# Optimization experiments

Hardware: AMD Instinct MI355X
Metric: run time of the kernel (lower is better)

## Reference

```python
import jax, jax.numpy as jnp
import numpy as np
from jax import lax

EOS_ID = 2
START_ID = 1
NEG = -1e9
BEAM = 4
OUT_LEN = 48


def _lstm_gates(z):
    i, f, g, o = jnp.split(z, 4, axis=-1)
    return jax.nn.sigmoid(i), jax.nn.sigmoid(f), jnp.tanh(g), jax.nn.sigmoid(o)


def setup_inputs() -> dict:
    V, E, H, A = 32000, 512, 512, 512
    B, S_IN = 32, 128
    key = jax.random.key(0)
    ks = jax.random.split(key, 16)
    sd = 0.05
    n = lambda k, shp: jax.random.normal(k, shp, dtype=jnp.float32) * sd
    return {
        "encoder_inputs": jax.random.randint(ks[0], (B, S_IN), 0, V, dtype=jnp.int32),
        "decoder_inputs": jax.random.randint(ks[1], (B, OUT_LEN), 0, V, dtype=jnp.int32),
        "enc_emb": n(ks[2], (V, E)),
        "dec_emb": n(ks[3], (V, E)),
        "W_enc": n(ks[4], (E, 4 * H)),
        "U_enc": n(ks[5], (H, 4 * H)),
        "b_enc": jnp.zeros((4 * H,), jnp.float32),
        "W_dec": n(ks[6], (E + A, 4 * H)),
        "U_dec": n(ks[7], (H, 4 * H)),
        "b_dec": jnp.zeros((4 * H,), jnp.float32),
        "W_mem": n(ks[8], (H, A)),      # LuongAttention memory layer (no bias)
        "W_attn": n(ks[9], (2 * H, A)), # AttentionWrapper attention layer (no bias)
        "W_out": n(ks[10], (A, V)),
        "b_out": jnp.zeros((V,), jnp.float32),
    }


def reference(encoder_inputs, decoder_inputs, enc_emb, dec_emb, W_enc, U_enc, b_enc,
              W_dec, U_dec, b_dec, W_mem, W_attn, W_out, b_out):
    B = encoder_inputs.shape[0]
    H = U_enc.shape[0]
    A = W_mem.shape[1]
    V = W_out.shape[1]

    # ---- encoder LSTM (Keras gate order i,f,g,o) ----
    x = enc_emb[encoder_inputs]  # [B,S,E]
    def enc_step(carry, xt):
        h, c = carry
        i, f, g, o = _lstm_gates(xt @ W_enc + h @ U_enc + b_enc)
        c = f * c + i * g
        h = o * jnp.tanh(c)
        return (h, c), h
    h0 = jnp.zeros((B, H), x.dtype)
    (hN, cN), enc_out = lax.scan(enc_step, (h0, h0), x.transpose(1, 0, 2))
    enc_out = enc_out.transpose(1, 0, 2)       # [B,S,H] = attention values
    keys_mem = enc_out @ W_mem                 # [B,S,A] = attention keys

    # ---- beam search init (tile encoder final state over beams) ----
    h = jnp.broadcast_to(hN[:, None], (B, BEAM, H))
    c = jnp.broadcast_to(cN[:, None], (B, BEAM, H))
    attn = jnp.zeros((B, BEAM, A), x.dtype)
    cum = jnp.full((B, BEAM), NEG, x.dtype).at[:, 0].set(0.0)
    finished = jnp.zeros((B, BEAM), bool)
    tok = jnp.full((B, BEAM), START_ID, jnp.int32)
    eos_lp = jnp.full((V,), NEG, x.dtype).at[EOS_ID].set(0.0)

    def dec_step(carry, _):
        h, c, attn, cum, finished, tok = carry
        xe = dec_emb[tok]                                     # [B,K,E]
        inp = jnp.concatenate([xe, attn], axis=-1)            # cell_input_fn: concat(input, attention)
        i, f, g, o = _lstm_gates(inp @ W_dec + h @ U_dec + b_dec)
        c_new = f * c + i * g
        cell_out = o * jnp.tanh(c_new)                        # [B,K,H]
        scores = jnp.einsum('bkh,bsh->bks', cell_out, keys_mem)  # Luong dot score
        align = jax.nn.softmax(scores, axis=-1)
        ctx = jnp.einsum('bks,bsh->bkh', align, enc_out)
        attn_new = jnp.concatenate([cell_out, ctx], axis=-1) @ W_attn  # attention layer
        logits = attn_new @ W_out + b_out                     # [B,K,V]
        lp = jax.nn.log_softmax(logits, axis=-1)
        lp = jnp.where(finished[..., None], eos_lp, lp)       # finished beams repeat EOS
        total = cum[..., None] + lp
        vals, idx = lax.top_k(total.reshape(B, -1), BEAM)     # over K*V candidates
        parent = idx // V
        new_tok = (idx % V).astype(jnp.int32)
        g3 = lambda t: jnp.take_along_axis(t, parent[..., None], axis=1)
        h2 = g3(cell_out)
        c2 = g3(c_new)
        attn2 = g3(attn_new)
        fin = jnp.take_along_axis(finished, parent, axis=1) | (new_tok == EOS_ID)
        return (h2, c2, attn2, vals, fin, new_tok), (parent, new_tok)

    _, (parents, toks) = lax.scan(dec_step, (h, c, attn, cum, finished, tok), None, length=OUT_LEN)

    # ---- gather_tree: backtrack beam ancestry ----
    def back(ptr, pt):
        p, t = pt
        sel = jnp.take_along_axis(t, ptr, axis=1)
        return jnp.take_along_axis(p, ptr, axis=1), sel
    ptr0 = jnp.broadcast_to(jnp.arange(BEAM, dtype=jnp.int32)[None], (B, BEAM))
    _, pred = lax.scan(back, ptr0, (parents, toks), reverse=True)
    return pred.transpose(1, 0, 2)  # predicted_ids [B, T, beam]
```

## Files before the change

### kernel.cpp

```cpp
#include <hip/hip_runtime.h>
#include <math.h>

#define EOS_ID 2
#define START_ID 1
#define NEGV (-1e9f)

__device__ __forceinline__ float sigmoidf_(float x) { return 1.f / (1.f + expf(-x)); }

__device__ __forceinline__ void merge4_(float lv[4], int lc[4],
                                        const float rv[4], const int rc[4]) {
    float ov[4]; int oc[4];
    int ai = 0, bi = 0;
    #pragma unroll
    for (int o = 0; o < 4; o++) {
        const float avv = (ai == 0) ? lv[0] : (ai == 1) ? lv[1] : (ai == 2) ? lv[2] : lv[3];
        const int   acc = (ai == 0) ? lc[0] : (ai == 1) ? lc[1] : (ai == 2) ? lc[2] : lc[3];
        const float bvv = (bi == 0) ? rv[0] : (bi == 1) ? rv[1] : (bi == 2) ? rv[2] : rv[3];
        const int   bcc = (bi == 0) ? rc[0] : (bi == 1) ? rc[1] : (bi == 2) ? rc[2] : rc[3];
        const bool ta = (avv > bvv) || (avv == bvv && acc < bcc);
        ov[o] = ta ? avv : bvv;
        oc[o] = ta ? acc : bcc;
        if (ta) ai++; else bi++;
    }
    #pragma unroll
    for (int o = 0; o < 4; o++) { lv[o] = ov[o]; lc[o] = oc[o]; }
}

__device__ __forceinline__ void lse_combine_(float& m, float& s, float m2, float s2) {
    const float M = fmaxf(m, m2);
    s = s * expf(m - M) + s2 * expf(m2 - M);
    m = M;
}

template<int BM, int BN, int BK, int AMODE, int TRANS>
__global__ void __launch_bounds__(256) gemm_k(
    const float* __restrict__ A, const float* __restrict__ B,
    const float* __restrict__ bias, float* __restrict__ C,
    int M, int N, int K, const int* __restrict__ tokp)
{
    static_assert(BN == 64, "");
    constexpr int TM = BM / 16, TN = BN / 16;
    __shared__ __align__(16) float As[BK][BM];
    __shared__ __align__(16) float Bs[BK][BN];
    const int tid = threadIdx.x;
    const int n0 = blockIdx.x * BN, m0 = blockIdx.y * BM;
    const int tx = tid & 15, ty = tid >> 4;
    (void)M;

    float acc[TM][TN];
    #pragma unroll
    for (int i = 0; i < TM; i++)
        #pragma unroll
        for (int j = 0; j < TN; j++) acc[i][j] = 0.f;

    constexpr int A4 = BM * BK / 4;
    const bool aP = (A4 >= 256) || (tid < A4);
    const int am = tid / (BK / 4), ak4 = tid % (BK / 4);
    const int bk = tid >> 4, bn4 = tid & 15;

    const float* aRow = nullptr;
    if (aP) {
        if (AMODE == 0) {
            aRow = A + (size_t)(m0 + am) * K;
        } else {
            const int r = m0 + am;
            const int s = r >> 5, bidx = r & 31;
            aRow = A + (size_t)tokp[bidx * 128 + s] * 512;
        }
    }

    float4 aPF{}, bPF;
    if (aP) aPF = *reinterpret_cast<const float4*>(aRow + ak4 * 4);
    bPF = *reinterpret_cast<const float4*>(B + (size_t)bk * N + n0 + bn4 * 4);

    for (int k0 = 0; k0 < K; k0 += BK) {
        if (aP) {
            As[ak4 * 4 + 0][am] = aPF.x;
            As[ak4 * 4 + 1][am] = aPF.y;
            As[ak4 * 4 + 2][am] = aPF.z;
            As[ak4 * 4 + 3][am] = aPF.w;
        }
        *reinterpret_cast<float4*>(&Bs[bk][bn4 * 4]) = bPF;
        __syncthreads();
        const int kn = k0 + BK;
        if (kn < K) {
            if (aP) aPF = *reinterpret_cast<const float4*>(aRow + kn + ak4 * 4);
            bPF = *reinterpret_cast<const float4*>(B + (size_t)(kn + bk) * N + n0 + bn4 * 4);
        }
        #pragma unroll
        for (int kk = 0; kk < BK; kk++) {
            float af[TM], bf[TN];
            if constexpr (TM == 4) {
                const float4 t4 = *reinterpret_cast<const float4*>(&As[kk][ty * TM]);
                af[0] = t4.x; af[1] = t4.y; af[2] = t4.z; af[3] = t4.w;
            } else if constexpr (TM == 2) {
                const float2 t2 = *reinterpret_cast<const float2*>(&As[kk][ty * TM]);
                af[0] = t2.x; af[1] = t2.y;
            } else {
                af[0] = As[kk][ty];
            }
            const float4 b4 = *reinterpret_cast<const float4*>(&Bs[kk][tx * TN]);
            bf[0] = b4.x; bf[1] = b4.y; bf[2] = b4.z; bf[3] = b4.w;
            #pragma unroll
            for (int i = 0; i < TM; i++)
                #pragma unroll
                for (int j = 0; j < TN; j++) acc[i][j] += af[i] * bf[j];
        }
        __syncthreads();
    }

    if constexpr (TRANS) {
        #pragma unroll
        for (int i = 0; i < TM; i++) {
            const int r = m0 + ty * TM + i;
            const int b = r >> 7, s = r & 127;
            #pragma unroll
            for (int j = 0; j < TN; j++)
                C[((size_t)b * 512 + (n0 + tx * TN + j)) * 128 + s] = acc[i][j];
        }
    } else {
        float bv[TN];
        #pragma unroll
        for (int j = 0; j < TN; j++) bv[j] = bias ? bias[n0 + tx * TN + j] : 0.f;
        #pragma unroll
        for (int i = 0; i < TM; i++) {
            float4 o;
            o.x = acc[i][0] + bv[0]; o.y = acc[i][1] + bv[1];
            o.z = acc[i][2] + bv[2]; o.w = acc[i][3] + bv[3];
            *reinterpret_cast<float4*>(C + (size_t)(m0 + ty * TM + i) * N + n0 + tx * TN) = o;
        }
    }
}

__global__ void __launch_bounds__(256) pack_dec_k(
    const float* __restrict__ W_dec, const float* __restrict__ U_dec,
    const float* __restrict__ b_dec, float* __restrict__ Bp, float* __restrict__ bp,
    float* __restrict__ enc_c, float* __restrict__ hzero)
{
    const int idx = blockIdx.x * 256 + threadIdx.x;
    if (idx < 1536 * 2048) {
        const int k = idx >> 11, cp = idx & 2047;
        const int j = cp >> 2, g = cp & 3;
        const int sc = g * 512 + j;
        Bp[idx] = (k < 1024) ? W_dec[(size_t)k * 2048 + sc]
                             : U_dec[(size_t)(k - 1024) * 2048 + sc];
        if (idx < 2048) bp[idx] = b_dec[sc];
    }
    if (idx < 32 * 512) enc_c[idx] = 0.f;
    if (idx < 512) hzero[idx] = 0.f;
}

__global__ void __launch_bounds__(256) enc_step_k(
    const float* __restrict__ Xz_t, const float* __restrict__ hprev, long hstride,
    const float* __restrict__ U, float* __restrict__ c, float* __restrict__ hout)
{
    __shared__ __align__(16) float hs[512][2];
    __shared__ __align__(16) float zp[8][2][128];
    __shared__ float zfin[2][32][4];
    const int tid = threadIdx.x;
    const int jt = blockIdx.x;
    const int b0 = blockIdx.y * 2;

    {
        const int bb = tid >> 7, k4 = tid & 127;
        const float4 hv = *reinterpret_cast<const float4*>(
            hprev + (size_t)(b0 + bb) * hstride + k4 * 4);
        hs[k4 * 4 + 0][bb] = hv.x; hs[k4 * 4 + 1][bb] = hv.y;
        hs[k4 * 4 + 2][bb] = hv.z; hs[k4 * 4 + 3][bb] = hv.w;
    }
    __syncthreads();

    {
        const int kp = tid >> 5, cq = tid & 31;
        const int g = cq >> 3, j4 = (cq & 7) * 4;
        const int col = g * 512 + jt * 32 + j4;
        const int kbase = kp * 64;
        float4 A0 = {0.f, 0.f, 0.f, 0.f}, A1 = {0.f, 0.f, 0.f, 0.f};
        #pragma unroll 8
        for (int k = 0; k < 64; k++) {
            const float4 u4 = *reinterpret_cast<const float4*>(
                U + (size_t)(kbase + k) * 2048 + col);
            const float2 h2 = *reinterpret_cast<const float2*>(&hs[kbase + k][0]);
            A0.x += h2.x * u4.x; A0.y += h2.x * u4.y;
            A0.z += h2.x * u4.z; A0.w += h2.x * u4.w;
            A1.x += h2.y * u4.x; A1.y += h2.y * u4.y;
            A1.z += h2.y * u4.z; A1.w += h2.y * u4.w;
        }
        *reinterpret_cast<float4*>(&zp[kp][0][g * 32 + j4]) = A0;
        *reinterpret_cast<float4*>(&zp[kp][1][g * 32 + j4]) = A1;
    }
    __syncthreads();

    {
        const int bb = tid >> 7, rem = tid & 127;
        const int jj = rem >> 2, gg = rem & 3;
        float s = 0.f;
        #pragma unroll
        for (int p = 0; p < 8; p++) s += zp[p][bb][gg * 32 + jj];
        s += Xz_t[(size_t)(b0 + bb) * 2048 + gg * 512 + jt * 32 + jj];
        zfin[bb][jj][gg] = s;
    }
    __syncthreads();

    if (tid < 64) {
        const int bb = tid >> 5, jj = tid & 31;
        const int b = b0 + bb;
        const float iv = sigmoidf_(zfin[bb][jj][0]);
        const float fv = sigmoidf_(zfin[bb][jj][1]);
        const float gv = tanhf(zfin[bb][jj][2]);
        const float ov = sigmoidf_(zfin[bb][jj][3]);
        const int jglob = jt * 32 + jj;
        const size_t ci = (size_t)b * 512 + jglob;
        const float cv = fv * c[ci] + iv * gv;
        c[ci] = cv;
        hout[(size_t)b * 128 * 512 + jglob] = ov * tanhf(cv);
    }
}

__global__ void __launch_bounds__(256) init_dec_k(
    const float* __restrict__ enc_out, const float* __restrict__ enc_c,
    float* __restrict__ h_buf, float* __restrict__ c_buf, float* __restrict__ attn_buf,
    float* __restrict__ cum, int* __restrict__ fin, int* __restrict__ tok)
{
    const int idx = blockIdx.x * 256 + threadIdx.x;
    const int r = idx >> 9, jcol = idx & 511;
    const int b = r >> 2, kbeam = r & 3;
    h_buf[idx] = enc_out[((size_t)b * 128 + 127) * 512 + jcol];
    c_buf[idx] = enc_c[(size_t)b * 512 + jcol];
    attn_buf[idx] = 0.f;
    if (jcol == 0) {
        cum[r] = (kbeam == 0) ? 0.f : NEGV;
        fin[r] = 0;
        tok[r] = START_ID;
    }
}

__global__ void __launch_bounds__(256) zgemm_gates_k(
    const float* __restrict__ dec_emb, const float* __restrict__ Bp,
    const float* __restrict__ bp, const int* __restrict__ tok,
    const float* __restrict__ attn_buf, const float* __restrict__ h_buf,
    const float* __restrict__ c_buf, float* __restrict__ c_new,
    float* __restrict__ Acat)
{
    constexpr int BK = 16;
    __shared__ __align__(16) float As[BK][16];
    __shared__ __align__(16) float Bs[BK][64];
    const int tid = threadIdx.x;
    const int n0 = blockIdx.x * 64, m0 = blockIdx.y * 16;
    const int tx = tid & 15, ty = tid >> 4;

    float acc[4] = {0.f, 0.f, 0.f, 0.f};

    const bool aP = tid < 64;
    const int am = tid >> 2, ak4 = tid & 3;
    const int r = m0 + am;
    const int bk = tid >> 4, bn4 = tid & 15;
    const float* embRow = aP ? (dec_emb + (size_t)tok[r] * 512) : nullptr;

    auto loadA = [&](int k0) -> float4 {
        const int kg = k0 + ak4 * 4;
        if (kg < 512)
            return *reinterpret_cast<const float4*>(embRow + kg);
        if (kg < 1024)
            return *reinterpret_cast<const float4*>(attn_buf + (size_t)r * 512 + (kg - 512));
        return *reinterpret_cast<const float4*>(h_buf + (size_t)r * 512 + (kg - 1024));
    };

    float4 aPF{}, bPF;
    if (aP) aPF = loadA(0);
    bPF = *reinterpret_cast<const float4*>(Bp + (size_t)bk * 2048 + n0 + bn4 * 4);

    for (int k0 = 0; k0 < 1536; k0 += BK) {
        if (aP) {
            As[ak4 * 4 + 0][am] = aPF.x;
            As[ak4 * 4 + 1][am] = aPF.y;
            As[ak4 * 4 + 2][am] = aPF.z;
            As[ak4 * 4 + 3][am] = aPF.w;
        }
        *reinterpret_cast<float4*>(&Bs[bk][bn4 * 4]) = bPF;
        __syncthreads();
        const int kn = k0 + BK;
        if (kn < 1536) {
            if (aP) aPF = loadA(kn);
            bPF = *reinterpret_cast<const float4*>(Bp + (size_t)(kn + bk) * 2048 + n0 + bn4 * 4);
        }
        #pragma unroll
        for (int kk = 0; kk < BK; kk++) {
            const float a = As[kk][ty];
            const float4 b4 = *reinterpret_cast<const float4*>(&Bs[kk][tx * 4]);
            acc[0] += a * b4.x; acc[1] += a * b4.y;
            acc[2] += a * b4.z; acc[3] += a * b4.w;
        }
        __syncthreads();
    }

    const int rr = m0 + ty;
    const int j = (n0 >> 2) + tx;
    const float iv = sigmoidf_(acc[0] + bp[n0 + tx * 4 + 0]);
    const float fv = sigmoidf_(acc[1] + bp[n0 + tx * 4 + 1]);
    const float gv = tanhf   (acc[2] + bp[n0 + tx * 4 + 2]);
    const float ov = sigmoidf_(acc[3] + bp[n0 + tx * 4 + 3]);
    const float cv = fv * c_buf[(size_t)rr * 512 + j] + iv * gv;
    c_new[(size_t)rr * 512 + j] = cv;
    Acat[(size_t)rr * 1024 + j] = ov * tanhf(cv);
}

__global__ void __launch_bounds__(256) attention_k(
    const float* __restrict__ Acat, const float* __restrict__ keysT,
    const float* __restrict__ enc_out, float* __restrict__ AcatW)
{
    __shared__ __align__(16) float q[512];
    __shared__ float scp[2][128];
    __shared__ float sc[128];
    __shared__ float red[128];
    const int r = blockIdx.x;
    const int b = r >> 2;
    const int tid = threadIdx.x;

    if (tid < 128)
        reinterpret_cast<float4*>(q)[tid] =
            reinterpret_cast<const float4*>(Acat + (size_t)r * 1024)[tid];
    __syncthreads();

    {
        const int half = tid >> 7, s = tid & 127;
        const float* kp = keysT + ((size_t)b * 512 + half * 256) * 128 + s;
        float acc = 0.f;
        #pragma unroll 8
        for (int kk = 0; kk < 256; kk++) acc += q[half * 256 + kk] * kp[(size_t)kk * 128];
        scp[half][s] = acc;
    }
    __syncthreads();
    if (tid < 128) sc[tid] = scp[0][tid] + scp[1][tid];
    __syncthreads();
    if (tid < 64) red[tid] = fmaxf(sc[tid], sc[tid + 64]);
    __syncthreads();
    for (int st = 32; st >= 1; st >>= 1) {
        if (tid < st) red[tid] = fmaxf(red[tid], red[tid + st]);
        __syncthreads();
    }
    const float m = red[0];
    __syncthreads();
    if (tid < 128) sc[tid] = expf(sc[tid] - m);
    __syncthreads();
    if (tid < 64) red[tid] = sc[tid] + sc[tid + 64];
    __syncthreads();
    for (int st = 32; st >= 1; st >>= 1) {
        if (tid < st) red[tid] += red[tid + st];
        __syncthreads();
    }
    const float S = red[0];
    __syncthreads();
    if (tid < 128) sc[tid] = sc[tid] / S;
    __syncthreads();

    float a0 = 0.f, a1 = 0.f;
    for (int s = 0; s < 128; s++) {
        const float w = sc[s];
        const float* vr = enc_out + ((size_t)b * 128 + s) * 512;
        a0 += w * vr[tid];
        a1 += w * vr[tid + 256];
    }
    AcatW[(size_t)r * 1024 + 512 + tid] = a0;
    AcatW[(size_t)r * 1024 + 512 + tid + 256] = a1;
}

__global__ void __launch_bounds__(256) logits_top_k(
    const float* __restrict__ A, const float* __restrict__ B,
    const float* __restrict__ bias, float* __restrict__ pmax,
    float* __restrict__ psum, float* __restrict__ pval, int* __restrict__ pcol)
{
    constexpr int BK = 16;
    __shared__ __align__(16) float As[BK][128];
    __shared__ __align__(16) float Bs[BK][64];
    const int tid = threadIdx.x;
    const int n0 = blockIdx.x * 64;
    const int t = blockIdx.x;
    const int tx = tid & 15, ty = tid >> 4;

    float acc[8][4];
    #pragma unroll
    for (int i = 0; i < 8; i++)
        #pragma unroll
        for (int j = 0; j < 4; j++) acc[i][j] = 0.f;

    const int amA = tid >> 2, ak4 = tid & 3;
    const int bkB = tid >> 4, bn4 = tid & 15;

    float4 aPF0 = *reinterpret_cast<const float4*>(A + (size_t)amA * 512 + ak4 * 4);
    float4 aPF1 = *reinterpret_cast<const float4*>(A + (size_t)(64 + amA) * 512 + ak4 * 4);
    float4 bPF  = *reinterpret_cast<const float4*>(B + (size_t)bkB * 32000 + n0 + bn4 * 4);

    for (int k0 = 0; k0 < 512; k0 += BK) {
        As[ak4 * 4 + 0][amA] = aPF0.x;
        As[ak4 * 4 + 1][amA] = aPF0.y;
        As[ak4 * 4 + 2][amA] = aPF0.z;
        As[ak4 * 4 + 3][amA] = aPF0.w;
        As[ak4 * 4 + 0][64 + amA] = aPF1.x;
        As[ak4 * 4 + 1][64 + amA] = aPF1.y;
        As[ak4 * 4 + 2][64 + amA] = aPF1.z;
        As[ak4 * 4 + 3][64 + amA] = aPF1.w;
        *reinterpret_cast<float4*>(&Bs[bkB][bn4 * 4]) = bPF;
        __syncthreads();
        const int kn = k0 + BK;
        if (kn < 512) {
            aPF0 = *reinterpret_cast<const float4*>(A + (size_t)amA * 512 + kn + ak4 * 4);
            aPF1 = *reinterpret_cast<const float4*>(A + (size_t)(64 + amA) * 512 + kn + ak4 * 4);
            bPF  = *reinterpret_cast<const float4*>(B + (size_t)(kn + bkB) * 32000 + n0 + bn4 * 4);
        }
        #pragma unroll
        for (int kk = 0; kk < BK; kk++) {
            float af[8];
            const float4 t0 = *reinterpret_cast<const float4*>(&As[kk][ty * 8]);
            const float4 t1 = *reinterpret_cast<const float4*>(&As[kk][ty * 8 + 4]);
            af[0] = t0.x; af[1] = t0.y; af[2] = t0.z; af[3] = t0.w;
            af[4] = t1.x; af[5] = t1.y; af[6] = t1.z; af[7] = t1.w;
            const float4 b4 = *reinterpret_cast<const float4*>(&Bs[kk][tx * 4]);
            #pragma unroll
            for (int i = 0; i < 8; i++) {
                acc[i][0] += af[i] * b4.x; acc[i][1] += af[i] * b4.y;
                acc[i][2] += af[i] * b4.z; acc[i][3] += af[i] * b4.w;
            }
        }
        __syncthreads();
    }

    float bv[4];
    #pragma unroll
    for (int j = 0; j < 4; j++) bv[j] = bias[n0 + tx * 4 + j];

    #pragma unroll
    for (int i = 0; i < 8; i++) {
        const int r = ty * 8 + i;
        float lv[4]; int lc[4];
        #pragma unroll
        for (int j = 0; j < 4; j++) { lv[j] = acc[i][j] + bv[j]; lc[j] = n0 + tx * 4 + j; }
        float rm = fmaxf(fmaxf(lv[0], lv[1]), fmaxf(lv[2], lv[3]));
        #pragma unroll
        for (int d = 1; d <= 8; d <<= 1) rm = fmaxf(rm, __shfl_xor(rm, d));
        float s4 = expf(lv[0] - rm) + expf(lv[1] - rm) + expf(lv[2] - rm) + expf(lv[3] - rm);
        #pragma unroll
        for (int d = 1; d <= 8; d <<= 1) s4 += __shfl_xor(s4, d);
        #pragma unroll
        for (int p = 0; p < 3; p++)
            #pragma unroll
            for (int q = 0; q < 3 - p; q++)
                if (lv[q + 1] > lv[q]) {
                    const float tv = lv[q]; lv[q] = lv[q + 1]; lv[q + 1] = tv;
                    const int tc = lc[q]; lc[q] = lc[q + 1]; lc[q + 1] = tc;
                }
        #pragma unroll
        for (int d = 1; d <= 8; d <<= 1) {
            float rv[4]; int rc[4];
            #pragma unroll
            for (int j = 0; j < 4; j++) {
                rv[j] = __shfl_xor(lv[j], d);
                rc[j] = __shfl_xor(lc[j], d);
            }
            merge4_(lv, lc, rv, rc);
        }
        if (tx == 0) {
            pmax[r * 512 + t] = rm;
            psum[r * 512 + t] = s4;
            #pragma unroll
            for (int j = 0; j < 4; j++) {
                pval[(r * 4 + j) * 512 + t] = lv[j];
                pcol[(r * 4 + j) * 512 + t] = lc[j];
            }
        }
    }
}

__global__ void __launch_bounds__(1024) merge_update_k(
    const float* __restrict__ pmax, const float* __restrict__ psum,
    const float* __restrict__ pval, const int* __restrict__ pcol,
    float* __restrict__ cum, int* __restrict__ fin, int* __restrict__ tok,
    const float* __restrict__ Acat, const float* __restrict__ c_new,
    const float* __restrict__ attn_new,
    float* __restrict__ h_buf, float* __restrict__ c_buf, float* __restrict__ attn_buf,
    int* __restrict__ parents_t, int* __restrict__ toks_t)
{
    const int b = blockIdx.x;
    const int tid = threadIdx.x;
    const int rloc = tid >> 8, lt = tid & 255;
    const int r = b * 4 + rloc;

    __shared__ float sm[4][256], ss[4][256];
    __shared__ float sv[4][256][4];
    __shared__ int   sc4[4][256][4];
    __shared__ float rowlse[4], rowv[4][4];
    __shared__ int   rowc[4][4];
    __shared__ float oldcum[4];
    __shared__ int   oldfin[4], par[4];

    if (tid < 4) {
        oldcum[tid] = cum[b * 4 + tid];
        oldfin[tid] = fin[b * 4 + tid];
    }

    float m = -INFINITY, s = 0.f;
    float lv[4] = {-INFINITY, -INFINITY, -INFINITY, -INFINITY};
    int lc[4] = {0x7FFFFFFF, 0x7FFFFFFF, 0x7FFFFFFF, 0x7FFFFFFF};
    for (int t = lt; t < 500; t += 256) {
        lse_combine_(m, s, pmax[r * 512 + t], psum[r * 512 + t]);
        float rv[4]; int rc[4];
        #pragma unroll
        for (int j = 0; j < 4; j++) {
            rv[j] = pval[(r * 4 + j) * 512 + t];
            rc[j] = pcol[(r * 4 + j) * 512 + t];
        }
        merge4_(lv, lc, rv, rc);
    }
    sm[rloc][lt] = m; ss[rloc][lt] = s;
    #pragma unroll
    for (int j = 0; j < 4; j++) { sv[rloc][lt][j] = lv[j]; sc4[rloc][lt][j] = lc[j]; }
    __syncthreads();

    for (int st = 128; st >= 1; st >>= 1) {
        if (lt < st) {
            float m2 = sm[rloc][lt + st], s2 = ss[rloc][lt + st];
            lse_combine_(m, s, m2, s2);
            sm[rloc][lt] = m; ss[rloc][lt] = s;
            float rv[4]; int rc[4];
            #pragma unroll
            for (int j = 0; j < 4; j++) {
                rv[j] = sv[rloc][lt + st][j];
                rc[j] = sc4[rloc][lt + st][j];
            }
            merge4_(lv, lc, rv, rc);
            #pragma unroll
            for (int j = 0; j < 4; j++) { sv[rloc][lt][j] = lv[j]; sc4[rloc][lt][j] = lc[j]; }
        }
        __syncthreads();
    }
    if (lt == 0) {
        rowlse[rloc] = m + logf(s);
        #pragma unroll
        for (int j = 0; j < 4; j++) { rowv[rloc][j] = lv[j]; rowc[rloc][j] = lc[j]; }
    }
    __syncthreads();

    if (tid == 0) {
        float cv[16]; int ci[16];
        const int fillv[3] = {0, 1, 3};
        for (int k = 0; k < 4; k++) {
            if (oldfin[k]) {
                cv[k * 4 + 0] = oldcum[k];
                ci[k * 4 + 0] = k * 32000 + EOS_ID;
                for (int j = 1; j < 4; j++) {
                    cv[k * 4 + j] = oldcum[k] + NEGV;
                    ci[k * 4 + j] = k * 32000 + fillv[j - 1];
                }
            } else {
                const float lse = rowlse[k];
                for (int j = 0; j < 4; j++) {
                    cv[k * 4 + j] = oldcum[k] + (rowv[k][j] - lse);
                    ci[k * 4 + j] = k * 32000 + rowc[k][j];
                }
            }
        }
        for (int rr = 0; rr < 4; rr++) {
            float bvv = -INFINITY; int bix = 0x7FFFFFFF, bp_ = -1;
            for (int q = 0; q < 16; q++) {
                if (cv[q] > bvv || (cv[q] == bvv && ci[q] < bix)) {
                    bvv = cv[q]; bix = ci[q]; bp_ = q;
                }
            }
            cv[bp_] = -INFINITY; ci[bp_] = 0x7FFFFFFF;
            const int k = bix / 32000, v = bix - k * 32000;
            par[rr] = k;
            parents_t[b * 4 + rr] = k;
            toks_t[b * 4 + rr] = v;
            cum[b * 4 + rr] = bvv;
            tok[b * 4 + rr] = v;
            fin[b * 4 + rr] = (oldfin[k] || v == EOS_ID) ? 1 : 0;
        }
    }
    __syncthreads();

    for (int idx = tid; idx < 4 * 512; idx += 1024) {
        const int j = idx >> 9, col = idx & 511;
        const int sr = b * 4 + par[j], dr = b * 4 + j;
        h_buf[(size_t)dr * 512 + col] = Acat[(size_t)sr * 1024 + col];
        c_buf[(size_t)dr * 512 + col] = c_new[(size_t)sr * 512 + col];
        attn_buf[(size_t)dr * 512 + col] = attn_new[(size_t)sr * 512 + col];
    }
}

__global__ void __launch_bounds__(128) backtrack_k(
    const int* __restrict__ parents, const int* __restrict__ toks,
    int* __restrict__ out)
{
    const int tid = threadIdx.x;
    const int b = tid >> 2, kc = tid & 3;
    int ptr = kc;
    for (int t = 47; t >= 0; --t) {
        out[b * 192 + t * 4 + kc] = toks[t * 128 + b * 4 + ptr];
        ptr = parents[t * 128 + b * 4 + ptr];
    }
}

extern "C" void kernel_launch(void* const* d_in, const int* in_sizes, int n_in,
                              void* d_out, int out_size, void* d_ws, size_t ws_size,
                              hipStream_t stream)
{
    (void)in_sizes; (void)n_in; (void)out_size; (void)ws_size;
    const int* enc_in = (const int*)d_in[0];
    const float* enc_emb = (const float*)d_in[2];
    const float* dec_emb = (const float*)d_in[3];
    const float* W_enc = (const float*)d_in[4];
    const float* U_enc = (const float*)d_in[5];
    const float* b_enc = (const float*)d_in[6];
    const float* W_dec = (const float*)d_in[7];
    const float* U_dec = (const float*)d_in[8];
    const float* b_dec = (const float*)d_in[9];
    const float* W_mem = (const float*)d_in[10];
    const float* W_attn = (const float*)d_in[11];
    const float* W_out = (const float*)d_in[12];
    const float* b_out = (const float*)d_in[13];
    int* out = (int*)d_out;

    char* ws = (char*)d_ws;
    size_t off = 0;
    auto alloc = [&](size_t bytes) -> char* {
        char* p = ws + off;
        off = (off + bytes + 255) & ~(size_t)255;
        return p;
    };
    float* Xz       = (float*)alloc(128ull * 32 * 2048 * 4);
    float* enc_out  = (float*)alloc(32ull * 128 * 512 * 4);
    float* keysT    = (float*)alloc(32ull * 512 * 128 * 4);
    float* Bp       = (float*)alloc(1536ull * 2048 * 4);
    float* bp       = (float*)alloc(2048 * 4);
    float* enc_c    = (float*)alloc(32ull * 512 * 4);
    float* hzero    = (float*)alloc(512 * 4);
    float* h_buf    = (float*)alloc(128ull * 512 * 4);
    float* c_buf    = (float*)alloc(128ull * 512 * 4);
    float* attn_buf = (float*)alloc(128ull * 512 * 4);
    float* c_new    = (float*)alloc(128ull * 512 * 4);
    float* Acat     = (float*)alloc(128ull * 1024 * 4);
    float* attn_new = (float*)alloc(128ull * 512 * 4);
    float* pmax     = (float*)alloc(128ull * 512 * 4);
    float* psum     = (float*)alloc(128ull * 512 * 4);
    float* pval     = (float*)alloc(512ull * 512 * 4);
    int*   pcol     = (int*)alloc(512ull * 512 * 4);
    float* cum      = (float*)alloc(128 * 4);
    int* fin        = (int*)alloc(128 * 4);
    int* tok        = (int*)alloc(128 * 4);
    int* parents    = (int*)alloc(48 * 128 * 4);
    int* toks       = (int*)alloc(48 * 128 * 4);

    pack_dec_k<<<(1536 * 2048) / 256, 256, 0, stream>>>(W_dec, U_dec, b_dec, Bp, bp,
                                                        enc_c, hzero);

    gemm_k<64, 64, 16, 2, 0><<<dim3(32, 64), 256, 0, stream>>>(
        enc_emb, W_enc, b_enc, Xz, 4096, 2048, 512, enc_in);

    for (int t = 0; t < 128; t++) {
        const float* hprev = t ? (enc_out + (size_t)(t - 1) * 512) : hzero;
        const long hstride = t ? (long)(128 * 512) : 0;
        enc_step_k<<<dim3(16, 16), 256, 0, stream>>>(
            Xz + (size_t)t * 32 * 2048, hprev, hstride, U_enc, enc_c,
            enc_out + (size_t)t * 512);
    }

    gemm_k<64, 64, 16, 0, 1><<<dim3(8, 64), 256, 0, stream>>>(
        enc_out, W_mem, nullptr, keysT, 4096, 512, 512, nullptr);

    init_dec_k<<<256, 256, 0, stream>>>(enc_out, enc_c, h_buf, c_buf, attn_buf,
                                        cum, fin, tok);

    for (int t = 0; t < 48; t++) {
        zgemm_gates_k<<<dim3(32, 8), 256, 0, stream>>>(
            dec_emb, Bp, bp, tok, attn_buf, h_buf, c_buf, c_new, Acat);
        attention_k<<<128, 256, 0, stream>>>(Acat, keysT, enc_out, Acat);
        gemm_k<16, 64, 16, 0, 0><<<dim3(8, 8), 256, 0, stream>>>(
            Acat, W_attn, nullptr, attn_new, 128, 512, 1024, nullptr);
        logits_top_k<<<500, 256, 0, stream>>>(
            attn_new, W_out, b_out, pmax, psum, pval, pcol);
        merge_update_k<<<32, 1024, 0, stream>>>(
            pmax, psum, pval, pcol, cum, fin, tok, Acat, c_new, attn_new,
            h_buf, c_buf, attn_buf, parents + t * 128, toks + t * 128);
    }

    backtrack_k<<<1, 128, 0, stream>>>(parents, toks, out);
}
```

Measured before the change: 10.87 ms.

## Fuse attention projection into attention kernel and gather beam state lazily via parent indices

Each decoder step now folds the W_attn projection into the attention kernel, so one launch per step goes away along with the Acat round trip through memory. Beam reordering no longer copies h, c and attn rows in merge_update. Instead it records each beam's parent index, and the next step's gates kernel reads from the parent rows in ping-pong buffers. The cost is that the fused projection runs only 128 blocks, each streaming the full 1024x512 W_attn from cache, which may be slower than the tiled GEMM it replaces.

```diff
diff --git a/kernel.cpp b/kernel.cpp
--- a/kernel.cpp
+++ b/kernel.cpp
@@ -193,12 +193,12 @@
 
     {
         const int bb = tid >> 7, rem = tid & 127;
-        const int jj = rem >> 2, gg = rem & 3;
+        const int jj = rem >> 2, gg2 = rem & 3;
         float s = 0.f;
         #pragma unroll
-        for (int p = 0; p < 8; p++) s += zp[p][bb][gg * 32 + jj];
-        s += Xz_t[(size_t)(b0 + bb) * 2048 + gg * 512 + jt * 32 + jj];
-        zfin[bb][jj][gg] = s;
+        for (int p = 0; p < 8; p++) s += zp[p][bb][gg2 * 32 + jj];
+        s += Xz_t[(size_t)(b0 + bb) * 2048 + gg2 * 512 + jt * 32 + jj];
+        zfin[bb][jj][gg2] = s;
     }
     __syncthreads();
 
@@ -219,28 +219,31 @@
 
 __global__ void __launch_bounds__(256) init_dec_k(
     const float* __restrict__ enc_out, const float* __restrict__ enc_c,
-    float* __restrict__ h_buf, float* __restrict__ c_buf, float* __restrict__ attn_buf,
-    float* __restrict__ cum, int* __restrict__ fin, int* __restrict__ tok)
+    float* __restrict__ ho_p, float* __restrict__ c_p, float* __restrict__ at_p,
+    float* __restrict__ cum, int* __restrict__ fin, int* __restrict__ tok,
+    int* __restrict__ parc)
 {
     const int idx = blockIdx.x * 256 + threadIdx.x;
     const int r = idx >> 9, jcol = idx & 511;
     const int b = r >> 2, kbeam = r & 3;
-    h_buf[idx] = enc_out[((size_t)b * 128 + 127) * 512 + jcol];
-    c_buf[idx] = enc_c[(size_t)b * 512 + jcol];
-    attn_buf[idx] = 0.f;
+    ho_p[idx] = enc_out[((size_t)b * 128 + 127) * 512 + jcol];
+    c_p[idx] = enc_c[(size_t)b * 512 + jcol];
+    at_p[idx] = 0.f;
     if (jcol == 0) {
         cum[r] = (kbeam == 0) ? 0.f : NEGV;
         fin[r] = 0;
         tok[r] = START_ID;
+        parc[r] = kbeam;
     }
 }
 
 __global__ void __launch_bounds__(256) zgemm_gates_k(
     const float* __restrict__ dec_emb, const float* __restrict__ Bp,
     const float* __restrict__ bp, const int* __restrict__ tok,
-    const float* __restrict__ attn_buf, const float* __restrict__ h_buf,
-    const float* __restrict__ c_buf, float* __restrict__ c_new,
-    float* __restrict__ Acat)
+    const int* __restrict__ parc,
+    const float* __restrict__ at_p, const float* __restrict__ ho_p,
+    const float* __restrict__ c_p, float* __restrict__ c_c,
+    float* __restrict__ ho_c)
 {
     constexpr int BK = 16;
     __shared__ __align__(16) float As[BK][16];
@@ -255,15 +258,20 @@
     const int am = tid >> 2, ak4 = tid & 3;
     const int r = m0 + am;
     const int bk = tid >> 4, bn4 = tid & 15;
-    const float* embRow = aP ? (dec_emb + (size_t)tok[r] * 512) : nullptr;
+    const float* embRow = nullptr;
+    int sr = 0;
+    if (aP) {
+        embRow = dec_emb + (size_t)tok[r] * 512;
+        sr = (r & ~3) | parc[r];
+    }
 
     auto loadA = [&](int k0) -> float4 {
         const int kg = k0 + ak4 * 4;
         if (kg < 512)
             return *reinterpret_cast<const float4*>(embRow + kg);
         if (kg < 1024)
-            return *reinterpret_cast<const float4*>(attn_buf + (size_t)r * 512 + (kg - 512));
-        return *reinterpret_cast<const float4*>(h_buf + (size_t)r * 512 + (kg - 1024));
+            return *reinterpret_cast<const float4*>(at_p + (size_t)sr * 512 + (kg - 512));
+        return *reinterpret_cast<const float4*>(ho_p + (size_t)sr * 512 + (kg - 1024));
     };
 
     float4 aPF{}, bPF;
@@ -295,21 +303,23 @@
     }
 
     const int rr = m0 + ty;
+    const int sre = (rr & ~3) | parc[rr];
     const int j = (n0 >> 2) + tx;
     const float iv = sigmoidf_(acc[0] + bp[n0 + tx * 4 + 0]);
     const float fv = sigmoidf_(acc[1] + bp[n0 + tx * 4 + 1]);
     const float gv = tanhf   (acc[2] + bp[n0 + tx * 4 + 2]);
     const float ov = sigmoidf_(acc[3] + bp[n0 + tx * 4 + 3]);
-    const float cv = fv * c_buf[(size_t)rr * 512 + j] + iv * gv;
-    c_new[(size_t)rr * 512 + j] = cv;
-    Acat[(size_t)rr * 1024 + j] = ov * tanhf(cv);
-}
-
-__global__ void __launch_bounds__(256) attention_k(
-    const float* __restrict__ Acat, const float* __restrict__ keysT,
-    const float* __restrict__ enc_out, float* __restrict__ AcatW)
-{
-    __shared__ __align__(16) float q[512];
+    const float cv = fv * c_p[(size_t)sre * 512 + j] + iv * gv;
+    c_c[(size_t)rr * 512 + j] = cv;
+    ho_c[(size_t)rr * 512 + j] = ov * tanhf(cv);
+}
+
+__global__ void __launch_bounds__(256) attn_fused_k(
+    const float* __restrict__ ho_c, const float* __restrict__ keysT,
+    const float* __restrict__ enc_out, const float* __restrict__ W_attn,
+    float* __restrict__ at_c)
+{
+    __shared__ __align__(16) float q[1024];
     __shared__ float scp[2][128];
     __shared__ float sc[128];
     __shared__ float red[128];
@@ -319,7 +329,7 @@
 
     if (tid < 128)
         reinterpret_cast<float4*>(q)[tid] =
-            reinterpret_cast<const float4*>(Acat + (size_t)r * 1024)[tid];
+            reinterpret_cast<const float4*>(ho_c + (size_t)r * 512)[tid];
     __syncthreads();
 
     {
@@ -354,15 +364,33 @@
     if (tid < 128) sc[tid] = sc[tid] / S;
     __syncthreads();
 
-    float a0 = 0.f, a1 = 0.f;
-    for (int s = 0; s < 128; s++) {
-        const float w = sc[s];
-        const float* vr = enc_out + ((size_t)b * 128 + s) * 512;
-        a0 += w * vr[tid];
-        a1 += w * vr[tid + 256];
-    }
-    AcatW[(size_t)r * 1024 + 512 + tid] = a0;
-    AcatW[(size_t)r * 1024 + 512 + tid + 256] = a1;
+    {
+        float a0 = 0.f, a1 = 0.f;
+        for (int s = 0; s < 128; s++) {
+            const float w = sc[s];
+            const float* vr = enc_out + ((size_t)b * 128 + s) * 512;
+            a0 += w * vr[tid];
+            a1 += w * vr[tid + 256];
+        }
+        q[512 + tid] = a0;
+        q[512 + 256 + tid] = a1;
+    }
+    __syncthreads();
+
+    {
+        const int n = tid * 2;
+        float acc0 = 0.f, acc1 = 0.f;
+        const float* wp = W_attn + n;
+        #pragma unroll 8
+        for (int k = 0; k < 1024; k++) {
+            const float2 w2 = *reinterpret_cast<const float2*>(wp + (size_t)k * 512);
+            const float a = q[k];
+            acc0 += a * w2.x;
+            acc1 += a * w2.y;
+        }
+        float2 o; o.x = acc0; o.y = acc1;
+        *reinterpret_cast<float2*>(at_c + (size_t)r * 512 + n) = o;
+    }
 }
 
 __global__ void __launch_bounds__(256) logits_top_k(
@@ -475,9 +503,7 @@
     const float* __restrict__ pmax, const float* __restrict__ psum,
     const float* __restrict__ pval, const int* __restrict__ pcol,
     float* __restrict__ cum, int* __restrict__ fin, int* __restrict__ tok,
-    const float* __restrict__ Acat, const float* __restrict__ c_new,
-    const float* __restrict__ attn_new,
-    float* __restrict__ h_buf, float* __restrict__ c_buf, float* __restrict__ attn_buf,
+    int* __restrict__ parc,
     int* __restrict__ parents_t, int* __restrict__ toks_t)
 {
     const int b = blockIdx.x;
@@ -491,7 +517,7 @@
     __shared__ float rowlse[4], rowv[4][4];
     __shared__ int   rowc[4][4];
     __shared__ float oldcum[4];
-    __shared__ int   oldfin[4], par[4];
+    __shared__ int   oldfin[4];
 
     if (tid < 4) {
         oldcum[tid] = cum[b * 4 + tid];
@@ -568,22 +594,13 @@
             }
             cv[bp_] = -INFINITY; ci[bp_] = 0x7FFFFFFF;
             const int k = bix / 32000, v = bix - k * 32000;
-            par[rr] = k;
+            parc[b * 4 + rr] = k;
             parents_t[b * 4 + rr] = k;
             toks_t[b * 4 + rr] = v;
             cum[b * 4 + rr] = bvv;
             tok[b * 4 + rr] = v;
             fin[b * 4 + rr] = (oldfin[k] || v == EOS_ID) ? 1 : 0;
         }
-    }
-    __syncthreads();
-
-    for (int idx = tid; idx < 4 * 512; idx += 1024) {
-        const int j = idx >> 9, col = idx & 511;
-        const int sr = b * 4 + par[j], dr = b * 4 + j;
-        h_buf[(size_t)dr * 512 + col] = Acat[(size_t)sr * 1024 + col];
-        c_buf[(size_t)dr * 512 + col] = c_new[(size_t)sr * 512 + col];
-        attn_buf[(size_t)dr * 512 + col] = attn_new[(size_t)sr * 512 + col];
     }
 }
 
@@ -634,12 +651,12 @@
     float* bp       = (float*)alloc(2048 * 4);
     float* enc_c    = (float*)alloc(32ull * 512 * 4);
     float* hzero    = (float*)alloc(512 * 4);
-    float* h_buf    = (float*)alloc(128ull * 512 * 4);
-    float* c_buf    = (float*)alloc(128ull * 512 * 4);
-    float* attn_buf = (float*)alloc(128ull * 512 * 4);
-    float* c_new    = (float*)alloc(128ull * 512 * 4);
-    float* Acat     = (float*)alloc(128ull * 1024 * 4);
-    float* attn_new = (float*)alloc(128ull * 512 * 4);
+    float* ho0      = (float*)alloc(128ull * 512 * 4);
+    float* ho1      = (float*)alloc(128ull * 512 * 4);
+    float* c0       = (float*)alloc(128ull * 512 * 4);
+    float* c1       = (float*)alloc(128ull * 512 * 4);
+    float* at0      = (float*)alloc(128ull * 512 * 4);
+    float* at1      = (float*)alloc(128ull * 512 * 4);
     float* pmax     = (float*)alloc(128ull * 512 * 4);
     float* psum     = (float*)alloc(128ull * 512 * 4);
     float* pval     = (float*)alloc(512ull * 512 * 4);
@@ -647,8 +664,13 @@
     float* cum      = (float*)alloc(128 * 4);
     int* fin        = (int*)alloc(128 * 4);
     int* tok        = (int*)alloc(128 * 4);
+    int* parc       = (int*)alloc(128 * 4);
     int* parents    = (int*)alloc(48 * 128 * 4);
     int* toks       = (int*)alloc(48 * 128 * 4);
+
+    float* hoB[2] = {ho0, ho1};
+    float* cB[2]  = {c0, c1};
+    float* atB[2] = {at0, at1};
 
     pack_dec_k<<<(1536 * 2048) / 256, 256, 0, stream>>>(W_dec, U_dec, b_dec, Bp, bp,
                                                         enc_c, hzero);
@@ -667,20 +689,21 @@
     gemm_k<64, 64, 16, 0, 1><<<dim3(8, 64), 256, 0, stream>>>(
         enc_out, W_mem, nullptr, keysT, 4096, 512, 512, nullptr);
 
-    init_dec_k<<<256, 256, 0, stream>>>(enc_out, enc_c, h_buf, c_buf, attn_buf,
-                                        cum, fin, tok);
+    init_dec_k<<<256, 256, 0, stream>>>(enc_out, enc_c, hoB[0], cB[0], atB[0],
+                                        cum, fin, tok, parc);
 
     for (int t = 0; t < 48; t++) {
+        const int p = t & 1;
+        const int c = p ^ 1;
         zgemm_gates_k<<<dim3(32, 8), 256, 0, stream>>>(
-            dec_emb, Bp, bp, tok, attn_buf, h_buf, c_buf, c_new, Acat);
-        attention_k<<<128, 256, 0, stream>>>(Acat, keysT, enc_out, Acat);
-        gemm_k<16, 64, 16, 0, 0><<<dim3(8, 8), 256, 0, stream>>>(
-            Acat, W_attn, nullptr, attn_new, 128, 512, 1024, nullptr);
+            dec_emb, Bp, bp, tok, parc, atB[p], hoB[p], cB[p], cB[c], hoB[c]);
+        attn_fused_k<<<128, 256, 0, stream>>>(
+            hoB[c], keysT, enc_out, W_attn, atB[c]);
         logits_top_k<<<500, 256, 0, stream>>>(
-            attn_new, W_out, b_out, pmax, psum, pval, pcol);
+            atB[c], W_out, b_out, pmax, psum, pval, pcol);
         merge_update_k<<<32, 1024, 0, stream>>>(
-            pmax, psum, pval, pcol, cum, fin, tok, Acat, c_new, attn_new,
-            h_buf, c_buf, attn_buf, parents + t * 128, toks + t * 128);
+            pmax, psum, pval, pcol, cum, fin, tok, parc,
+            parents + t * 128, toks + t * 128);
     }
 
     backtrack_k<<<1, 128, 0, stream>>>(parents, toks, out);
```

Result: slower. 11.49 ms (+5.8%).
